# Kernel optimization log

Hardware: AMD Instinct MI355X
Metric: run time of the kernel (lower is better)

The kernel has to match this reference:

```python
import jax, jax.numpy as jnp
import numpy as np

EPS = 1e-5  # BatchNorm2d default eps
NH, KD, HD = 8, 16, 32  # num_heads, key_dim, head_dim (dim=256, attn_ratio=0.5)


def _bn(y, g, b, m, v):
    # inference BatchNorm2d over channel axis 1
    s = g / jnp.sqrt(v + EPS)
    return y * s[None, :, None, None] + (b - m * s)[None, :, None, None]


def setup_inputs() -> dict:
    key = jax.random.key(0)
    ks = jax.random.split(key, 16)
    d = {}
    d['x'] = jax.random.normal(ks[0], (8, 256, 32, 32), jnp.float32)
    d['w_qkv'] = jax.random.normal(ks[1], (512, 256), jnp.float32) * 0.05
    d['qkv_g'] = jax.random.uniform(ks[2], (512,), jnp.float32, 0.5, 1.5)
    d['qkv_b'] = jax.random.normal(ks[3], (512,), jnp.float32) * 0.1
    d['qkv_m'] = jax.random.normal(ks[4], (512,), jnp.float32) * 0.1
    d['qkv_v'] = jax.random.uniform(ks[5], (512,), jnp.float32, 0.5, 1.5)
    d['w_pe'] = jax.random.normal(ks[6], (256, 1, 3, 3), jnp.float32) * 0.1
    d['pe_g'] = jax.random.uniform(ks[7], (256,), jnp.float32, 0.5, 1.5)
    d['pe_b'] = jax.random.normal(ks[8], (256,), jnp.float32) * 0.1
    d['pe_m'] = jax.random.normal(ks[9], (256,), jnp.float32) * 0.1
    d['pe_v'] = jax.random.uniform(ks[10], (256,), jnp.float32, 0.5, 1.5)
    d['w_proj'] = jax.random.normal(ks[11], (256, 256), jnp.float32) * 0.05
    d['proj_g'] = jax.random.uniform(ks[12], (256,), jnp.float32, 0.5, 1.5)
    d['proj_b'] = jax.random.normal(ks[13], (256,), jnp.float32) * 0.1
    d['proj_m'] = jax.random.normal(ks[14], (256,), jnp.float32) * 0.1
    d['proj_v'] = jax.random.uniform(ks[15], (256,), jnp.float32, 0.5, 1.5)
    return d


def reference(x, w_qkv, qkv_g, qkv_b, qkv_m, qkv_v,
              w_pe, pe_g, pe_b, pe_m, pe_v,
              w_proj, proj_g, proj_b, proj_m, proj_v):
    B, C, H, W = x.shape
    N = H * W
    scale = KD ** (-0.5)
    # qkv: 1x1 conv + BN
    qkv = _bn(jnp.einsum('bchw,oc->bohw', x, w_qkv), qkv_g, qkv_b, qkv_m, qkv_v)
    qkv = qkv.reshape(B, NH, 2 * KD + HD, N)
    q, k, v = qkv[:, :, :KD], qkv[:, :, KD:2 * KD], qkv[:, :, 2 * KD:]
    # attn[b,h,n,m] = sum_c q[b,h,c,n] k[b,h,c,m] * scale
    attn = jax.nn.softmax(jnp.einsum('bhcn,bhcm->bhnm', q, k) * scale, axis=-1)
    # out[b,h,c,n] = sum_m v[b,h,c,m] attn[b,h,n,m]
    out = jnp.einsum('bhcm,bhnm->bhcn', v, attn).reshape(B, C, H, W)
    # pe: depthwise 3x3 conv + BN on v reshaped to image layout
    pe_in = v.reshape(B, C, H, W)
    pe = jax.lax.conv_general_dilated(
        pe_in, w_pe, window_strides=(1, 1), padding='SAME',
        feature_group_count=C, dimension_numbers=('NCHW', 'OIHW', 'NCHW'))
    pe = _bn(pe, pe_g, pe_b, pe_m, pe_v)
    y = out + pe
    # proj: 1x1 conv + BN
    return _bn(jnp.einsum('bchw,oc->bohw', y, w_proj), proj_g, proj_b, proj_m, proj_v)
```

## Files before the change

kernel.cpp:

```cpp
#include <hip/hip_runtime.h>
#include <hip/hip_bf16.h>
#include <math.h>

#define EPS 1e-5f
#define QSCALE 0.36067376022224085f

typedef __attribute__((ext_vector_type(8))) short bf16x8;
typedef __attribute__((ext_vector_type(8))) unsigned short ushort8;
typedef __attribute__((ext_vector_type(16))) float f32x16;

__device__ inline float bf2f(unsigned short u) {
    unsigned int v = ((unsigned int)u) << 16;
    return __uint_as_float(v);
}
__device__ inline unsigned int pk2f(float a, float b) {
    unsigned int ua = __float_as_uint(a), ub = __float_as_uint(b);
    ua += 0x7fffu + ((ua >> 16) & 1u);
    ub += 0x7fffu + ((ub >> 16) & 1u);
    return (ua >> 16) | (ub & 0xffff0000u);
}

__global__ __launch_bounds__(256)
void qkv_gemm_kernel(const float* __restrict__ x, const float* __restrict__ w,
                     const float* __restrict__ g, const float* __restrict__ bbias,
                     const float* __restrict__ bmean, const float* __restrict__ bvar,
                     const float* __restrict__ wproj,
                     unsigned short* __restrict__ qt,
                     unsigned short* __restrict__ kt,
                     unsigned short* __restrict__ vt,
                     unsigned short* __restrict__ wpb)
{
    const int bx = blockIdx.x;
    const int b  = bx & 7;
    const int r  = bx >> 3;
    const int o0 = (r & 3) * 128;
    const int n0 = (r >> 2) * 64;

    const int tid = threadIdx.x;

    if (bx < 16) {
        const int t = bx * 256 + tid;
        const int base = t * 16;
        const int kb = base >> 11;
        const int o  = (base >> 3) & 255;
        const float* s0 = wproj + (size_t)o * 256 + kb * 8;
        float4 a0 = *(const float4*)s0;
        float4 a1 = *(const float4*)(s0 + 4);
        float4 a2 = *(const float4*)(s0 + 256);
        float4 a3 = *(const float4*)(s0 + 260);
        uint4 w0 = make_uint4(pk2f(a0.x, a0.y), pk2f(a0.z, a0.w), pk2f(a1.x, a1.y), pk2f(a1.z, a1.w));
        uint4 w1 = make_uint4(pk2f(a2.x, a2.y), pk2f(a2.z, a2.w), pk2f(a3.x, a3.y), pk2f(a3.z, a3.w));
        *(uint4*)(wpb + base) = w0;
        *(uint4*)(wpb + base + 8) = w1;
    }

    __shared__ unsigned short As[128][136];
    __shared__ unsigned short Bs[64][136];

    const int wid = tid >> 6;
    const int lane = tid & 63;
    const int col = lane & 31;
    const int h2 = lane >> 5;

    f32x16 acc0 = {}, acc1 = {};

    #pragma unroll
    for (int s = 0; s < 2; s++) {
        const int k0 = s * 128;
        __syncthreads();
        #pragma unroll
        for (int i = 0; i < 16; i++) {
            int flat = tid + i * 256;
            int row = flat >> 5;
            int kq  = flat & 31;
            float4 a4 = *(const float4*)&w[(size_t)(o0 + row) * 256 + k0 + kq * 4];
            *(uint2*)&As[row][kq * 4] = make_uint2(pk2f(a4.x, a4.y), pk2f(a4.z, a4.w));
        }
        const float* xb = x + (size_t)b * 256 * 1024;
        #pragma unroll
        for (int i = 0; i < 8; i++) {
            int flat = tid + i * 256;
            int c  = flat >> 4;
            int nq = flat & 15;
            float4 b4 = *(const float4*)&xb[(size_t)(k0 + c) * 1024 + n0 + nq * 4];
            unsigned int lo = pk2f(b4.x, b4.y), hi = pk2f(b4.z, b4.w);
            Bs[nq * 4 + 0][c] = (unsigned short)lo;
            Bs[nq * 4 + 1][c] = (unsigned short)(lo >> 16);
            Bs[nq * 4 + 2][c] = (unsigned short)hi;
            Bs[nq * 4 + 3][c] = (unsigned short)(hi >> 16);
        }
        __syncthreads();
        #pragma unroll
        for (int ks = 0; ks < 8; ks++) {
            bf16x8 af = *(bf16x8*)&As[wid * 32 + col][ks * 16 + 8 * h2];
            bf16x8 b0 = *(bf16x8*)&Bs[col][ks * 16 + 8 * h2];
            bf16x8 b1 = *(bf16x8*)&Bs[32 + col][ks * 16 + 8 * h2];
            acc0 = __builtin_amdgcn_mfma_f32_32x32x16_bf16(af, b0, acc0, 0, 0, 0);
            acc1 = __builtin_amdgcn_mfma_f32_32x32x16_bf16(af, b1, acc1, 0, 0, 0);
        }
    }

    #pragma unroll
    for (int gq = 0; gq < 4; gq++) {
        const int ob = o0 + wid * 32 + 8 * gq + 4 * h2;
        float4 gg = *(const float4*)&g[ob];
        float4 bb = *(const float4*)&bbias[ob];
        float4 mm = *(const float4*)&bmean[ob];
        float4 vv = *(const float4*)&bvar[ob];
        float sm[4], sa[4];
        sm[0] = gg.x * rsqrtf(vv.x + EPS); sa[0] = bb.x - mm.x * sm[0];
        sm[1] = gg.y * rsqrtf(vv.y + EPS); sa[1] = bb.y - mm.y * sm[1];
        sm[2] = gg.z * rsqrtf(vv.z + EPS); sa[2] = bb.z - mm.z * sm[2];
        sm[3] = gg.w * rsqrtf(vv.w + EPS); sa[3] = bb.w - mm.w * sm[3];

        #pragma unroll
        for (int t = 0; t < 2; t++) {
            const f32x16& ac = t ? acc1 : acc0;
            const int n = n0 + t * 32 + col;
            float val[4];
            #pragma unroll
            for (int j = 0; j < 4; j++) val[j] = ac[4 * gq + j] * sm[j] + sa[j];

            const int h  = (o0 >> 6) + (wid >> 1);
            const int bh = b * 8 + h;
            const int rb = 8 * gq + 4 * h2;
            if ((wid & 1) == 0) {
                const bool isq = (gq < 2);
                if (isq) {
                    #pragma unroll
                    for (int j = 0; j < 4; j++) val[j] *= QSCALE;
                }
                unsigned short* dst = (isq ? qt : kt)
                    + ((size_t)(bh * 1024 + n) * 16 + (rb & 15));
                *(uint2*)dst = make_uint2(pk2f(val[0], val[1]), pk2f(val[2], val[3]));
            } else {
                unsigned short* vb = vt + (size_t)bh * 32768 + (n >> 3) * 256 + (n & 7);
                unsigned int lo = pk2f(val[0], val[1]), hi = pk2f(val[2], val[3]);
                vb[(rb + 0) * 8] = (unsigned short)lo;
                vb[(rb + 1) * 8] = (unsigned short)(lo >> 16);
                vb[(rb + 2) * 8] = (unsigned short)hi;
                vb[(rb + 3) * 8] = (unsigned short)(hi >> 16);
            }
        }
    }
}

__global__ __launch_bounds__(512)
void fused_attn_pe_proj_kernel(const unsigned short* __restrict__ qt,
                               const unsigned short* __restrict__ kt,
                               const unsigned short* __restrict__ vt,
                               const unsigned short* __restrict__ wpb,
                               const float* __restrict__ wpe,
                               const float* __restrict__ pe_g, const float* __restrict__ pe_b,
                               const float* __restrict__ pe_m, const float* __restrict__ pe_v,
                               const float* __restrict__ pj_g, const float* __restrict__ pj_b,
                               const float* __restrict__ pj_m, const float* __restrict__ pj_v,
                               float* __restrict__ out)
{
    const int blk = blockIdx.x;
    const int b  = blk & 7;
    const int py = blk >> 3;
    const int tid = threadIdx.x;
    const int wid = tid >> 6;
    const int lane = tid & 63;
    const int col = lane & 31;
    const int h2 = lane >> 5;
    const int bh = b * 8 + wid;
    const int n0 = py * 32;

    __shared__ __align__(16) unsigned short conv_lds[8][32][104];
    __shared__ float wpe_lds[8][32][9];
    __shared__ float pebn_lds[8][32][2];
    __shared__ __align__(16) unsigned short y_lds[32][256];

    {
        const int c  = lane >> 1;
        const int ph = (lane & 1) * 48;
        const unsigned short* vb = vt + (size_t)bh * 32768 + c * 8;
        #pragma unroll
        for (int j = 0; j < 48; j += 8) {
            int idx = ph + j;
            int prow = py - 1 + (idx >> 5);
            int px8  = (idx >> 3) & 3;
            ushort8 v8 = {};
            if (prow >= 0 && prow < 32)
                v8 = *(const ushort8*)(vb + (prow * 4 + px8) * 256);
            *(ushort8*)&conv_lds[wid][c][idx] = v8;
        }
        if (lane < 32) {
            int ch = wid * 32 + lane;
            #pragma unroll
            for (int t = 0; t < 9; t++) wpe_lds[wid][lane][t] = wpe[ch * 9 + t];
            float s = pe_g[ch] * rsqrtf(pe_v[ch] + EPS);
            pebn_lds[wid][lane][0] = s;
            pebn_lds[wid][lane][1] = pe_b[ch] - pe_m[ch] * s;
        }
    }

    const bf16x8 qf = *(const bf16x8*)(qt + ((size_t)bh * 1024 + n0 + col) * 16 + h2 * 8);
    const unsigned short* ktb = kt + (size_t)bh * 1024 * 16;
    const unsigned short* vtb = vt + (size_t)bh * 32768 + h2 * 256 + col * 8;

    f32x16 acc = {};
    f32x16 cin;
    #pragma unroll
    for (int r = 0; r < 16; r++) cin[r] = 0.f;
    float lrun_h = 0.f;

    bf16x8 kf  = *(const bf16x8*)(ktb + (size_t)col * 16 + h2 * 8);
    bf16x8 vf0 = *(const bf16x8*)(vtb);
    bf16x8 vf1 = *(const bf16x8*)(vtb + 512);

    for (int j = 0; j < 32; j++) {
        f32x16 d = __builtin_amdgcn_mfma_f32_32x32x16_bf16(kf, qf, cin, 0, 0, 0);

        bf16x8 kfn, vf0n, vf1n;
        if (j < 31) {
            const int m1 = (j + 1) * 32;
            kfn  = *(const bf16x8*)(ktb + (size_t)(m1 + col) * 16 + h2 * 8);
            vf0n = *(const bf16x8*)(vtb + m1 * 32);
            vf1n = *(const bf16x8*)(vtb + m1 * 32 + 512);
        }

        float m0 = fmaxf(fmaxf(d[0], d[1]), d[2]);
        float m1_ = fmaxf(fmaxf(d[3], d[4]), d[5]);
        float m2 = fmaxf(fmaxf(d[6], d[7]), d[8]);
        float m3 = fmaxf(fmaxf(d[9], d[10]), d[11]);
        float m4 = fmaxf(fmaxf(d[12], d[13]), d[14]);
        float tmax = fmaxf(fmaxf(fmaxf(m0, m1_), fmaxf(m2, m3)), fmaxf(m4, d[15]));

        if (!__all(tmax <= 8.0f)) {
            float tfull = fmaxf(tmax, __shfl_xor(tmax, 32, 64));
            float corr = __builtin_amdgcn_exp2f(-tfull);
            #pragma unroll
            for (int r = 0; r < 16; r++) cin[r] -= tfull;
            #pragma unroll
            for (int r = 0; r < 16; r++) acc[r] *= corr;
            lrun_h *= corr;
            #pragma unroll
            for (int r = 0; r < 16; r++) d[r] -= tfull;
        }

        float p[16];
        #pragma unroll
        for (int r = 0; r < 16; r++) p[r] = __builtin_amdgcn_exp2f(d[r]);

        {
            float s0 = (p[0] + p[1]) + (p[2] + p[3]);
            float s1 = (p[4] + p[5]) + (p[6] + p[7]);
            float s2 = (p[8] + p[9]) + (p[10] + p[11]);
            float s3 = (p[12] + p[13]) + (p[14] + p[15]);
            lrun_h += (s0 + s1) + (s2 + s3);
        }

        unsigned int pw[8];
        #pragma unroll
        for (int gq = 0; gq < 4; gq++) {
            pw[2 * gq + 0] = pk2f(p[4 * gq + 0], p[4 * gq + 1]);
            pw[2 * gq + 1] = pk2f(p[4 * gq + 2], p[4 * gq + 3]);
        }
        unsigned int sw[8];
        #pragma unroll
        for (int i = 0; i < 8; i++) sw[i] = __shfl_xor((int)pw[i], 32, 64);

        uint4 bfw0, bfw1;
        if (h2 == 0) {
            bfw0 = make_uint4(pw[0], pw[1], sw[0], sw[1]);
            bfw1 = make_uint4(pw[4], pw[5], sw[4], sw[5]);
        } else {
            bfw0 = make_uint4(sw[2], sw[3], pw[2], pw[3]);
            bfw1 = make_uint4(sw[6], sw[7], pw[6], pw[7]);
        }
        acc = __builtin_amdgcn_mfma_f32_32x32x16_bf16(vf0, *(bf16x8*)&bfw0, acc, 0, 0, 0);
        acc = __builtin_amdgcn_mfma_f32_32x32x16_bf16(vf1, *(bf16x8*)&bfw1, acc, 0, 0, 0);

        kf = kfn; vf0 = vf0n; vf1 = vf1n;
    }

    const float lsum = lrun_h + __shfl_xor(lrun_h, 32, 64);
    const float inv = 1.f / lsum;

    #pragma unroll
    for (int r = 0; r < 16; r += 2) {
        const int c = (r & 3) + 8 * (r >> 2) + 4 * h2;
        float yv[2];
        #pragma unroll
        for (int u = 0; u < 2; u++) {
            const int cc = c + u;
            float a = 0.f;
            #pragma unroll
            for (int dy = 0; dy < 3; dy++) {
                float vm = (col == 0)  ? 0.f : bf2f(conv_lds[wid][cc][dy * 32 + col - 1]);
                float v0 = bf2f(conv_lds[wid][cc][dy * 32 + col]);
                float vp2 = (col == 31) ? 0.f : bf2f(conv_lds[wid][cc][dy * 32 + col + 1]);
                a += vm  * wpe_lds[wid][cc][dy * 3 + 0]
                   + v0  * wpe_lds[wid][cc][dy * 3 + 1]
                   + vp2 * wpe_lds[wid][cc][dy * 3 + 2];
            }
            yv[u] = acc[r + u] * inv + (a * pebn_lds[wid][cc][0] + pebn_lds[wid][cc][1]);
        }
        unsigned int packed = pk2f(yv[0], yv[1]);
        int byte = (col * 512 + (wid * 32 + c) * 2) ^ (col << 4);
        *(unsigned int*)((char*)y_lds + byte) = packed;
    }
    __syncthreads();

    f32x16 accp = {};
    #pragma unroll
    for (int ks = 0; ks < 16; ks++) {
        bf16x8 af = *(const bf16x8*)(wpb + (size_t)(2 * ks + h2) * 2048 + (wid * 32 + col) * 8);
        int byte = (col * 512 + ks * 32 + h2 * 16) ^ (col << 4);
        bf16x8 bfr = *(bf16x8*)((char*)y_lds + byte);
        accp = __builtin_amdgcn_mfma_f32_32x32x16_bf16(af, bfr, accp, 0, 0, 0);
    }

    #pragma unroll
    for (int gq = 0; gq < 4; gq++) {
        const int ob = wid * 32 + 8 * gq + 4 * h2;
        float4 gg = *(const float4*)&pj_g[ob];
        float4 bb = *(const float4*)&pj_b[ob];
        float4 mm = *(const float4*)&pj_m[ob];
        float4 vv = *(const float4*)&pj_v[ob];
        float sm[4], sa[4];
        sm[0] = gg.x * rsqrtf(vv.x + EPS); sa[0] = bb.x - mm.x * sm[0];
        sm[1] = gg.y * rsqrtf(vv.y + EPS); sa[1] = bb.y - mm.y * sm[1];
        sm[2] = gg.z * rsqrtf(vv.z + EPS); sa[2] = bb.z - mm.z * sm[2];
        sm[3] = gg.w * rsqrtf(vv.w + EPS); sa[3] = bb.w - mm.w * sm[3];
        #pragma unroll
        for (int j = 0; j < 4; j++)
            out[((size_t)b * 256 + ob + j) * 1024 + n0 + col] = accp[4 * gq + j] * sm[j] + sa[j];
    }
}

extern "C" void kernel_launch(void* const* d_in, const int* in_sizes, int n_in,
                              void* d_out, int out_size, void* d_ws, size_t ws_size,
                              hipStream_t stream)
{
    const float* x      = (const float*)d_in[0];
    const float* w_qkv  = (const float*)d_in[1];
    const float* qkv_g  = (const float*)d_in[2];
    const float* qkv_b  = (const float*)d_in[3];
    const float* qkv_m  = (const float*)d_in[4];
    const float* qkv_v  = (const float*)d_in[5];
    const float* w_pe   = (const float*)d_in[6];
    const float* pe_g   = (const float*)d_in[7];
    const float* pe_b   = (const float*)d_in[8];
    const float* pe_m   = (const float*)d_in[9];
    const float* pe_v   = (const float*)d_in[10];
    const float* w_proj = (const float*)d_in[11];
    const float* proj_g = (const float*)d_in[12];
    const float* proj_b = (const float*)d_in[13];
    const float* proj_m = (const float*)d_in[14];
    const float* proj_v = (const float*)d_in[15];

    float* out = (float*)d_out;
    unsigned short* qt  = (unsigned short*)d_ws;
    unsigned short* kt  = qt + (size_t)64 * 1024 * 16;
    unsigned short* vt  = kt + (size_t)64 * 1024 * 16;
    unsigned short* wpb = vt + (size_t)64 * 32768;

    qkv_gemm_kernel<<<dim3(512), 256, 0, stream>>>(
        x, w_qkv, qkv_g, qkv_b, qkv_m, qkv_v, w_proj, qt, kt, vt, wpb);

    fused_attn_pe_proj_kernel<<<dim3(256), 512, 0, stream>>>(
        qt, kt, vt, wpb,
        w_pe, pe_g, pe_b, pe_m, pe_v,
        proj_g, proj_b, proj_m, proj_v,
        out);
}
```

Measured before the change: 45.27 us.

## Split attention key range across two wave groups with LDS softmax merge

Doubles the fused attention block to 1024 threads. Each head now has two waves, and each processes half of the 1024 keys with its own online softmax. The partial max, sum and accumulator are merged through shared memory, like flash-decoding. The proj GEMM K dimension is also split between the two waves and reduced through LDS. This shortens the serial per-wave loop and raises the wave count on the 256-block grid. The cost is extra shared memory, two more block-wide barriers, and register pressure from the launch bound of (1024, 4).

```diff
diff --git a/kernel.cpp b/kernel.cpp
--- a/kernel.cpp
+++ b/kernel.cpp
@@ -145,7 +145,7 @@
     }
 }
 
-__global__ __launch_bounds__(512)
+__global__ __launch_bounds__(1024, 4)
 void fused_attn_pe_proj_kernel(const unsigned short* __restrict__ qt,
                                const unsigned short* __restrict__ kt,
                                const unsigned short* __restrict__ vt,
@@ -162,18 +162,23 @@
     const int py = blk >> 3;
     const int tid = threadIdx.x;
     const int wid = tid >> 6;
+    const int head = wid & 7;
+    const int ksplit = wid >> 3;
     const int lane = tid & 63;
     const int col = lane & 31;
     const int h2 = lane >> 5;
-    const int bh = b * 8 + wid;
+    const int bh = b * 8 + head;
     const int n0 = py * 32;
 
     __shared__ __align__(16) unsigned short conv_lds[8][32][104];
     __shared__ float wpe_lds[8][32][9];
     __shared__ float pebn_lds[8][32][2];
     __shared__ __align__(16) unsigned short y_lds[32][256];
-
-    {
+    __shared__ float cmb[8][64][17];
+    __shared__ float cmm[8][64];
+    __shared__ float cml[8][64];
+
+    if (ksplit == 0) {
         const int c  = lane >> 1;
         const int ph = (lane & 1) * 48;
         const unsigned short* vb = vt + (size_t)bh * 32768 + c * 8;
@@ -185,15 +190,15 @@
             ushort8 v8 = {};
             if (prow >= 0 && prow < 32)
                 v8 = *(const ushort8*)(vb + (prow * 4 + px8) * 256);
-            *(ushort8*)&conv_lds[wid][c][idx] = v8;
+            *(ushort8*)&conv_lds[head][c][idx] = v8;
         }
         if (lane < 32) {
-            int ch = wid * 32 + lane;
-            #pragma unroll
-            for (int t = 0; t < 9; t++) wpe_lds[wid][lane][t] = wpe[ch * 9 + t];
+            int ch = head * 32 + lane;
+            #pragma unroll
+            for (int t = 0; t < 9; t++) wpe_lds[head][lane][t] = wpe[ch * 9 + t];
             float s = pe_g[ch] * rsqrtf(pe_v[ch] + EPS);
-            pebn_lds[wid][lane][0] = s;
-            pebn_lds[wid][lane][1] = pe_b[ch] - pe_m[ch] * s;
+            pebn_lds[head][lane][0] = s;
+            pebn_lds[head][lane][1] = pe_b[ch] - pe_m[ch] * s;
         }
     }
 
@@ -207,15 +212,16 @@
     for (int r = 0; r < 16; r++) cin[r] = 0.f;
     float lrun_h = 0.f;
 
-    bf16x8 kf  = *(const bf16x8*)(ktb + (size_t)col * 16 + h2 * 8);
-    bf16x8 vf0 = *(const bf16x8*)(vtb);
-    bf16x8 vf1 = *(const bf16x8*)(vtb + 512);
-
-    for (int j = 0; j < 32; j++) {
+    const int j0 = ksplit * 16;
+    bf16x8 kf  = *(const bf16x8*)(ktb + (size_t)(j0 * 32 + col) * 16 + h2 * 8);
+    bf16x8 vf0 = *(const bf16x8*)(vtb + j0 * 1024);
+    bf16x8 vf1 = *(const bf16x8*)(vtb + j0 * 1024 + 512);
+
+    for (int j = j0; j < j0 + 16; j++) {
         f32x16 d = __builtin_amdgcn_mfma_f32_32x32x16_bf16(kf, qf, cin, 0, 0, 0);
 
         bf16x8 kfn, vf0n, vf1n;
-        if (j < 31) {
+        if (j < j0 + 15) {
             const int m1 = (j + 1) * 32;
             kfn  = *(const bf16x8*)(ktb + (size_t)(m1 + col) * 16 + h2 * 8);
             vf0n = *(const bf16x8*)(vtb + m1 * 32);
@@ -277,58 +283,88 @@
         kf = kfn; vf0 = vf0n; vf1 = vf1n;
     }
 
-    const float lsum = lrun_h + __shfl_xor(lrun_h, 32, 64);
-    const float inv = 1.f / lsum;
-
-    #pragma unroll
-    for (int r = 0; r < 16; r += 2) {
-        const int c = (r & 3) + 8 * (r >> 2) + 4 * h2;
-        float yv[2];
-        #pragma unroll
-        for (int u = 0; u < 2; u++) {
-            const int cc = c + u;
-            float a = 0.f;
-            #pragma unroll
-            for (int dy = 0; dy < 3; dy++) {
-                float vm = (col == 0)  ? 0.f : bf2f(conv_lds[wid][cc][dy * 32 + col - 1]);
-                float v0 = bf2f(conv_lds[wid][cc][dy * 32 + col]);
-                float vp2 = (col == 31) ? 0.f : bf2f(conv_lds[wid][cc][dy * 32 + col + 1]);
-                a += vm  * wpe_lds[wid][cc][dy * 3 + 0]
-                   + v0  * wpe_lds[wid][cc][dy * 3 + 1]
-                   + vp2 * wpe_lds[wid][cc][dy * 3 + 2];
+    const float lfull = lrun_h + __shfl_xor(lrun_h, 32, 64);
+    const float mown  = -cin[0];
+
+    if (ksplit == 1) {
+        #pragma unroll
+        for (int r = 0; r < 16; r++) cmb[head][lane][r] = acc[r];
+        cmm[head][lane] = mown;
+        cml[head][lane] = lfull;
+    }
+    __syncthreads();
+
+    if (ksplit == 0) {
+        float m2x = cmm[head][lane];
+        float l2x = cml[head][lane];
+        float M   = fmaxf(mown, m2x);
+        float w1  = __builtin_amdgcn_exp2f(mown - M);
+        float w2  = __builtin_amdgcn_exp2f(m2x - M);
+        float inv = 1.f / (lfull * w1 + l2x * w2);
+
+        #pragma unroll
+        for (int r = 0; r < 16; r += 2) {
+            const int c = (r & 3) + 8 * (r >> 2) + 4 * h2;
+            float yv[2];
+            #pragma unroll
+            for (int u = 0; u < 2; u++) {
+                const int cc = c + u;
+                float am = acc[r + u] * w1 + cmb[head][lane][r + u] * w2;
+                float a = 0.f;
+                #pragma unroll
+                for (int dy = 0; dy < 3; dy++) {
+                    float vm = (col == 0)  ? 0.f : bf2f(conv_lds[head][cc][dy * 32 + col - 1]);
+                    float v0 = bf2f(conv_lds[head][cc][dy * 32 + col]);
+                    float vp2 = (col == 31) ? 0.f : bf2f(conv_lds[head][cc][dy * 32 + col + 1]);
+                    a += vm  * wpe_lds[head][cc][dy * 3 + 0]
+                       + v0  * wpe_lds[head][cc][dy * 3 + 1]
+                       + vp2 * wpe_lds[head][cc][dy * 3 + 2];
+                }
+                yv[u] = am * inv + (a * pebn_lds[head][cc][0] + pebn_lds[head][cc][1]);
             }
-            yv[u] = acc[r + u] * inv + (a * pebn_lds[wid][cc][0] + pebn_lds[wid][cc][1]);
-        }
-        unsigned int packed = pk2f(yv[0], yv[1]);
-        int byte = (col * 512 + (wid * 32 + c) * 2) ^ (col << 4);
-        *(unsigned int*)((char*)y_lds + byte) = packed;
+            unsigned int packed = pk2f(yv[0], yv[1]);
+            int byte = (col * 512 + (head * 32 + c) * 2) ^ (col << 4);
+            *(unsigned int*)((char*)y_lds + byte) = packed;
+        }
     }
     __syncthreads();
 
     f32x16 accp = {};
     #pragma unroll
-    for (int ks = 0; ks < 16; ks++) {
-        bf16x8 af = *(const bf16x8*)(wpb + (size_t)(2 * ks + h2) * 2048 + (wid * 32 + col) * 8);
-        int byte = (col * 512 + ks * 32 + h2 * 16) ^ (col << 4);
+    for (int i = 0; i < 8; i++) {
+        int ks2 = ksplit * 8 + i;
+        bf16x8 af = *(const bf16x8*)(wpb + (size_t)(2 * ks2 + h2) * 2048 + (head * 32 + col) * 8);
+        int byte = (col * 512 + ks2 * 32 + h2 * 16) ^ (col << 4);
         bf16x8 bfr = *(bf16x8*)((char*)y_lds + byte);
         accp = __builtin_amdgcn_mfma_f32_32x32x16_bf16(af, bfr, accp, 0, 0, 0);
     }
 
-    #pragma unroll
-    for (int gq = 0; gq < 4; gq++) {
-        const int ob = wid * 32 + 8 * gq + 4 * h2;
-        float4 gg = *(const float4*)&pj_g[ob];
-        float4 bb = *(const float4*)&pj_b[ob];
-        float4 mm = *(const float4*)&pj_m[ob];
-        float4 vv = *(const float4*)&pj_v[ob];
-        float sm[4], sa[4];
-        sm[0] = gg.x * rsqrtf(vv.x + EPS); sa[0] = bb.x - mm.x * sm[0];
-        sm[1] = gg.y * rsqrtf(vv.y + EPS); sa[1] = bb.y - mm.y * sm[1];
-        sm[2] = gg.z * rsqrtf(vv.z + EPS); sa[2] = bb.z - mm.z * sm[2];
-        sm[3] = gg.w * rsqrtf(vv.w + EPS); sa[3] = bb.w - mm.w * sm[3];
-        #pragma unroll
-        for (int j = 0; j < 4; j++)
-            out[((size_t)b * 256 + ob + j) * 1024 + n0 + col] = accp[4 * gq + j] * sm[j] + sa[j];
+    if (ksplit == 1) {
+        #pragma unroll
+        for (int r = 0; r < 16; r++) cmb[head][lane][r] = accp[r];
+    }
+    __syncthreads();
+
+    if (ksplit == 0) {
+        #pragma unroll
+        for (int r = 0; r < 16; r++) accp[r] += cmb[head][lane][r];
+
+        #pragma unroll
+        for (int gq = 0; gq < 4; gq++) {
+            const int ob = head * 32 + 8 * gq + 4 * h2;
+            float4 gg = *(const float4*)&pj_g[ob];
+            float4 bb = *(const float4*)&pj_b[ob];
+            float4 mm = *(const float4*)&pj_m[ob];
+            float4 vv = *(const float4*)&pj_v[ob];
+            float sm[4], sa[4];
+            sm[0] = gg.x * rsqrtf(vv.x + EPS); sa[0] = bb.x - mm.x * sm[0];
+            sm[1] = gg.y * rsqrtf(vv.y + EPS); sa[1] = bb.y - mm.y * sm[1];
+            sm[2] = gg.z * rsqrtf(vv.z + EPS); sa[2] = bb.z - mm.z * sm[2];
+            sm[3] = gg.w * rsqrtf(vv.w + EPS); sa[3] = bb.w - mm.w * sm[3];
+            #pragma unroll
+            for (int j = 0; j < 4; j++)
+                out[((size_t)b * 256 + ob + j) * 1024 + n0 + col] = accp[4 * gq + j] * sm[j] + sa[j];
+        }
     }
 }
 
@@ -362,7 +398,7 @@
     qkv_gemm_kernel<<<dim3(512), 256, 0, stream>>>(
         x, w_qkv, qkv_g, qkv_b, qkv_m, qkv_v, w_proj, qt, kt, vt, wpb);
 
-    fused_attn_pe_proj_kernel<<<dim3(256), 512, 0, stream>>>(
+    fused_attn_pe_proj_kernel<<<dim3(256), 1024, 0, stream>>>(
         qt, kt, vt, wpb,
         w_pe, pe_g, pe_b, pe_m, pe_v,
         proj_g, proj_b, proj_m, proj_v,
```

New measurement: 43.48 us. 1.04x faster.
